# Kernel optimization log

Hardware: AMD Instinct MI355X
Metric: run time of the kernel (lower is better)

The kernel has to match this reference:

```python
import jax, jax.numpy as jnp
import numpy as np

B, S, D, HE, HD = 64, 256, 512, 512, 1024  # batch, seq_len, input_dim, hidden_enc, hidden_dec (=2*HE)


def _gru_cell(h, x, Wih, Whh, bih, bhh):
    # single PyTorch-convention GRU step; gate order [r, z, n]
    H = h.shape[-1]
    gi = x @ Wih.T + bih  # [B, 3H]
    gh = h @ Whh.T + bhh
    r = jax.nn.sigmoid(gi[:, :H] + gh[:, :H])
    z = jax.nn.sigmoid(gi[:, H:2 * H] + gh[:, H:2 * H])
    n = jnp.tanh(gi[:, 2 * H:] + r * gh[:, 2 * H:])
    return (1.0 - z) * n + z * h


def _gru_seq(x, Wih, Whh, bih, bhh):
    # x: [B, S, D] -> outputs [B, S, H], zero initial hidden (torch default)
    h0 = jnp.zeros((x.shape[0], Whh.shape[1]), x.dtype)
    def step(h, xt):
        hn = _gru_cell(h, xt, Wih, Whh, bih, bhh)
        return hn, hn
    _, ys = jax.lax.scan(step, h0, jnp.swapaxes(x, 0, 1))
    return jnp.swapaxes(ys, 0, 1)


def _bigru(x, pf, pb):
    fwd = _gru_seq(x, *pf)
    bwd = _gru_seq(x[:, ::-1], *pb)[:, ::-1]
    return jnp.concatenate([fwd, bwd], axis=-1)  # [B, S, 2H]


def setup_inputs() -> dict:
    key = jax.random.key(0)
    ks = iter(jax.random.split(key, 40))
    f = lambda *shape: (jax.random.normal(next(ks), shape, dtype=jnp.float32) * 0.05)
    inp = {
        'input': f(B, 1, S, D),
        'eps': f(B, S, 2 * HE),
    }
    # encoder mu / sigma bidirectional GRUs (forward + backward directions)
    for name in ['mu_f', 'mu_b', 'sg_f', 'sg_b']:
        inp[name + '_Wih'] = f(3 * HE, D)
        inp[name + '_Whh'] = f(3 * HE, HE)
        inp[name + '_bih'] = f(3 * HE)
        inp[name + '_bhh'] = f(3 * HE)
    # decoder GRU (input_dim -> hidden_dec)
    inp['dec_Wih'] = f(3 * HD, D)
    inp['dec_Whh'] = f(3 * HD, HD)
    inp['dec_bih'] = f(3 * HD)
    inp['dec_bhh'] = f(3 * HD)
    # attention Linear(D+HD, 1) and output Linear(HD, D)
    inp['attn_W'] = f(1, D + HD)
    inp['attn_b'] = f(1)
    inp['lin_W'] = f(D, HD)
    inp['lin_b'] = f(D)
    return inp


def reference(input, eps,
              mu_f_Wih, mu_f_Whh, mu_f_bih, mu_f_bhh,
              mu_b_Wih, mu_b_Whh, mu_b_bih, mu_b_bhh,
              sg_f_Wih, sg_f_Whh, sg_f_bih, sg_f_bhh,
              sg_b_Wih, sg_b_Whh, sg_b_bih, sg_b_bhh,
              dec_Wih, dec_Whh, dec_bih, dec_bhh,
              attn_W, attn_b, lin_W, lin_b):
    x = input[:, 0]  # squeeze -> [B, S, D]
    # encoder (dropout is identity at eval)
    mu = _bigru(x, (mu_f_Wih, mu_f_Whh, mu_f_bih, mu_f_bhh),
                   (mu_b_Wih, mu_b_Whh, mu_b_bih, mu_b_bhh))
    logvar = _bigru(x, (sg_f_Wih, sg_f_Whh, sg_f_bih, sg_f_bhh),
                       (sg_b_Wih, sg_b_Whh, sg_b_bih, sg_b_bhh))
    z = mu + eps * jnp.exp(0.5 * logvar)  # [B, S, HD]

    # attention score = Linear([x_t, hidden]); split into precomputed x-part + per-step hidden part
    sx = x @ attn_W[0, :D] + attn_b[0]  # [B, S]
    wah = attn_W[0, D:]                  # [HD]
    pos = jnp.arange(S)

    def step(carry, i):
        hidden, out = carry  # [B, HD], [B, D]
        scores = sx + (hidden @ wah)[:, None]          # [B, S]
        scores = jnp.where(pos[None, :] == i, -jnp.inf, scores)  # leave-one-out
        w = jax.nn.softmax(scores, axis=1)
        ctx = jnp.einsum('bs,bsh->bh', w, z)           # context = decoder init hidden
        h_new = _gru_cell(ctx, out, dec_Wih, dec_Whh, dec_bih, dec_bhh)
        o_new = h_new @ lin_W.T + lin_b
        return (h_new, o_new), o_new

    h0 = jnp.zeros((B, HD), x.dtype)
    o0 = jnp.zeros((B, D), x.dtype)
    _, rec = jax.lax.scan(step, (h0, o0), pos)
    reconstructed = jnp.swapaxes(rec, 0, 1)  # [B, S, D]
    return reconstructed, mu, logvar
```

## Files before the change

kernel.cpp:

```cpp
#include <hip/hip_runtime.h>
#include <hip/hip_bf16.h>

typedef __hip_bfloat16 bf16;
typedef __attribute__((ext_vector_type(8))) short s8v;
typedef __attribute__((ext_vector_type(4))) float f32x4;
typedef __attribute__((ext_vector_type(4))) int int4v;

#define NB 64
#define NS 256
#define ND 512
#define NHE 512
#define NHD 1024
#define NGE 1536
#define NGD 3072

static __device__ __forceinline__ float sigmf(float x){ return 1.0f/(1.0f+__expf(-x)); }
static __device__ __forceinline__ float b2f(unsigned short u){ return __uint_as_float(((unsigned int)u) << 16); }
static __device__ __forceinline__ unsigned short f2bu(float f){
    bf16 v = __float2bfloat16(f);
    return *reinterpret_cast<unsigned short*>(&v);
}
static __device__ __forceinline__ s8v cast8(int4v v){
    union { int4v i; s8v s; } u; u.i = v; return u.s;
}
static __device__ __forceinline__ void st2_llc(const void* p, unsigned int v){
    asm volatile("global_store_short %0, %1, off sc0 sc1"
                 :: "v"((unsigned long long)(uintptr_t)p), "v"(v) : "memory");
}

#define LOADX8(BASEP, A0,A1,A2,A3,A4,A5,A6,A7)                                   \
    asm volatile(                                                                \
        "global_load_dwordx4 %0, %8, off sc0 sc1\n\t"                            \
        "global_load_dwordx4 %1, %8, off offset:64 sc0 sc1\n\t"                  \
        "global_load_dwordx4 %2, %8, off offset:128 sc0 sc1\n\t"                 \
        "global_load_dwordx4 %3, %8, off offset:192 sc0 sc1\n\t"                 \
        "global_load_dwordx4 %4, %8, off offset:256 sc0 sc1\n\t"                 \
        "global_load_dwordx4 %5, %8, off offset:320 sc0 sc1\n\t"                 \
        "global_load_dwordx4 %6, %8, off offset:384 sc0 sc1\n\t"                 \
        "global_load_dwordx4 %7, %8, off offset:448 sc0 sc1\n\t"                 \
        "s_waitcnt vmcnt(0)"                                                     \
        : "=&v"(A0),"=&v"(A1),"=&v"(A2),"=&v"(A3),                               \
          "=&v"(A4),"=&v"(A5),"=&v"(A6),"=&v"(A7)                                \
        : "v"((unsigned long long)(uintptr_t)(BASEP)) : "memory");               \
    __builtin_amdgcn_sched_barrier(0);

static __device__ __forceinline__ void groupbar_flat(unsigned int* base, int step, int nwg){
    __syncthreads();
    if (threadIdx.x == 0){
        unsigned int old = __hip_atomic_fetch_add(base, 1u, __ATOMIC_RELAXED, __HIP_MEMORY_SCOPE_AGENT);
        if ((int)old == step*nwg - 1)
            __hip_atomic_store(base + 32, (unsigned int)step, __ATOMIC_RELAXED, __HIP_MEMORY_SCOPE_AGENT);
        while ((int)__hip_atomic_load(base + 32, __ATOMIC_RELAXED, __HIP_MEMORY_SCOPE_AGENT) < step)
            __builtin_amdgcn_s_sleep(1);
    }
    __syncthreads();
}
static __device__ __forceinline__ void groupbar_tree(unsigned int* base, int step, int leaf){
    __syncthreads();
    if (threadIdx.x == 0){
        unsigned int lo = __hip_atomic_fetch_add(base + leaf*32, 1u, __ATOMIC_RELAXED, __HIP_MEMORY_SCOPE_AGENT);
        if ((int)lo == step*8 - 1){
            unsigned int ro = __hip_atomic_fetch_add(base + 256, 1u, __ATOMIC_RELAXED, __HIP_MEMORY_SCOPE_AGENT);
            if ((int)ro == step*8 - 1)
                __hip_atomic_store(base + 288, (unsigned int)step, __ATOMIC_RELAXED, __HIP_MEMORY_SCOPE_AGENT);
        }
        while ((int)__hip_atomic_load(base + 288, __ATOMIC_RELAXED, __HIP_MEMORY_SCOPE_AGENT) < step)
            __builtin_amdgcn_s_sleep(1);
    }
    __syncthreads();
}

__global__ __launch_bounds__(256) void k_sx(const float* __restrict__ x,
                                            const float* __restrict__ attnW,
                                            const float* __restrict__ attnb,
                                            float* __restrict__ sx){
    int row = blockIdx.x*4 + (threadIdx.x>>6);
    int lane = threadIdx.x & 63;
    float s = 0.f;
    for (int d = lane; d < ND; d += 64) s += x[(size_t)row*ND + d]*attnW[d];
    #pragma unroll
    for (int off = 32; off; off >>= 1) s += __shfl_down(s, off, 64);
    if (lane == 0) sx[row] = s + attnb[0];
}

__global__ __launch_bounds__(256) void k_cvec(const float* __restrict__ dWih,
                                              const float* __restrict__ linb,
                                              const float* __restrict__ dbih,
                                              float* __restrict__ cvec){
    int row = blockIdx.x*4 + (threadIdx.x>>6);
    int lane = threadIdx.x & 63;
    float s = 0.f;
    for (int d = lane; d < ND; d += 64) s += dWih[(size_t)row*ND + d]*linb[d];
    #pragma unroll
    for (int off = 32; off; off >>= 1) s += __shfl_down(s, off, 64);
    if (lane == 0) cvec[row] = s + dbih[row];
}

__global__ __launch_bounds__(256) void k_softprep2(const float* __restrict__ sx,
                                                   float* __restrict__ esb,
                                                   float* __restrict__ Se){
    int b = blockIdx.x, s = threadIdx.x;
    __shared__ float red[256];
    float v = sx[b*NS + s];
    red[s] = v; __syncthreads();
    for (int off = 128; off; off >>= 1){ if (s < off) red[s] = fmaxf(red[s], red[s+off]); __syncthreads(); }
    float mx = red[0]; __syncthreads();
    float ev = __expf(v - mx);
    esb[s*NB + b] = ev;
    red[s] = ev; __syncthreads();
    for (int off = 128; off; off >>= 1){ if (s < off) red[s] += red[s+off]; __syncthreads(); }
    if (s == 0) Se[b] = red[0];
}

__global__ __launch_bounds__(256) void k_cvtW(const float* __restrict__ W, bf16* __restrict__ o){
    size_t i = ((size_t)blockIdx.x*256 + threadIdx.x)*4;
    float4 v = *(const float4*)(W + i);
    o[i+0] = __float2bfloat16(v.x);
    o[i+1] = __float2bfloat16(v.y);
    o[i+2] = __float2bfloat16(v.z);
    o[i+3] = __float2bfloat16(v.w);
}

__global__ __launch_bounds__(256) void k_zexp3(const bf16* __restrict__ hxh,
                                               const float* __restrict__ eps,
                                               bf16* __restrict__ z){
    int t  = blockIdx.x >> 4;
    int hb = blockIdx.x & 15;
    int dmu = hb >> 3;
    int jm0 = (hb & 7)*64;
    const unsigned short* hu = (const unsigned short*)hxh;
    __shared__ unsigned short zt[64][66];
    int tid = threadIdx.x;
    #pragma unroll
    for (int q = 0; q < 16; ++q){
        int bb = q*4 + (tid>>6);
        int hc = tid & 63;
        float mu = b2f(hu[(((size_t)(dmu*NS) + t)*64 + bb)*512 + jm0 + hc]);
        float lv = b2f(hu[(((size_t)((2+dmu)*NS) + t)*64 + bb)*512 + jm0 + hc]);
        float ep = eps[((size_t)bb*NS + t)*NHD + hb*64 + hc];
        zt[bb][hc] = f2bu(mu + ep*__expf(0.5f*lv));
    }
    __syncthreads();
    unsigned short* zu = (unsigned short*)z;
    int b = tid & 63;
    #pragma unroll
    for (int q = 0; q < 16; ++q){
        int hl = q*4 + (tid>>6);
        zu[((size_t)t*NHD + hb*64 + hl)*NB + b] = zt[b][hl];
    }
}

__global__ __launch_bounds__(256) void k_outT2(const bf16* __restrict__ hxh,
                                               float* __restrict__ outMu,
                                               float* __restrict__ outLv){
    int t  = blockIdx.x;
    int b0 = blockIdx.y*8;
    const unsigned short* hu = (const unsigned short*)hxh;
    int tid = threadIdx.x;
    #pragma unroll
    for (int q = 0; q < 16; ++q){
        int idx = q*256 + tid;
        int sel = idx >> 11;
        int rem = idx & 2047;
        int bb  = b0 + (rem >> 8);
        int h   = (rem & 255)*4;
        int dirn = (h >> 9) + sel*2;
        int j   = h & 511;
        ushort4 v = *(const ushort4*)(hu + (((size_t)(dirn*NS) + t)*64 + bb)*512 + j);
        float4 o;
        o.x = b2f(v.x); o.y = b2f(v.y); o.z = b2f(v.z); o.w = b2f(v.w);
        float* outp = sel ? outLv : outMu;
        *(float4*)(outp + ((size_t)bb*NS + t)*NHD + h) = o;
    }
}

__global__ __launch_bounds__(256) void k_T2(const bf16* __restrict__ z,
                                            const float* __restrict__ esb,
                                            float* __restrict__ T){
    int h = blockIdx.x;
    int b = threadIdx.x & 63;
    int sq = threadIdx.x >> 6;
    __shared__ float red[4][64];
    float acc = 0.f;
    #pragma unroll 8
    for (int s = sq*64; s < sq*64 + 64; ++s)
        acc += esb[s*NB + b]*__bfloat162float(z[((size_t)s*NHD + h)*NB + b]);
    red[sq][b] = acc; __syncthreads();
    if (sq == 0) T[h*NB + b] = red[0][b] + red[1][b] + red[2][b] + red[3][b];
}

__global__ __launch_bounds__(256) void k_ctx3(const bf16* __restrict__ z,
                                              const float* __restrict__ esb,
                                              const float* __restrict__ Se,
                                              const float* __restrict__ T,
                                              bf16* __restrict__ ctxT,
                                              bf16* __restrict__ ctxB){
    int i  = blockIdx.x >> 4;
    int hb = blockIdx.x & 15;
    int tid = threadIdx.x;
    int b  = tid & 63;
    __shared__ unsigned short tt[64][66];
    float ei  = esb[i*NB + b];
    float inv = 1.0f/(Se[b] - ei);
    #pragma unroll
    for (int q = 0; q < 16; ++q){
        int hl = q*4 + (tid>>6);
        int h = hb*64 + hl;
        float zv = __bfloat162float(z[((size_t)i*NHD + h)*NB + b]);
        float cv = (T[h*NB + b] - ei*zv)*inv;
        unsigned short u = f2bu(cv);
        ctxT[((size_t)i*NHD + h)*NB + b] = *reinterpret_cast<bf16*>(&u);
        tt[hl][b] = u;
    }
    __syncthreads();
    unsigned short* cb = (unsigned short*)ctxB;
    #pragma unroll
    for (int q = 0; q < 16; ++q){
        int bn = q*4 + (tid>>6);
        int hl = tid & 63;
        cb[((size_t)i*NB + bn)*NHD + hb*64 + hl] = tt[hl][bn];
    }
}

__global__ __launch_bounds__(256) void k_gemm_M(
    const float* __restrict__ dWih,
    const float* __restrict__ linW,
    bf16* __restrict__ M){
    int g0 = blockIdx.x*64;
    int h0 = blockIdx.y*64;
    __shared__ float As[64][36];
    __shared__ float Bs[32][68];
    int tid = threadIdx.x, tx = tid & 15, ty = tid >> 4;
    float acc[4][4] = {};
    for (int k0 = 0; k0 < ND; k0 += 32){
        #pragma unroll
        for (int m = 0; m < 8; ++m){
            int idx = m*256 + tid;
            int row = idx >> 5, kk = idx & 31;
            As[row][kk] = dWih[(size_t)(g0+row)*ND + k0 + kk];
            int k2 = idx >> 6, hh2 = idx & 63;
            Bs[k2][hh2] = linW[(size_t)(k0+k2)*NHD + h0 + hh2];
        }
        __syncthreads();
        for (int k = 0; k < 32; ++k){
            float a[4];
            #pragma unroll
            for (int i = 0; i < 4; ++i) a[i] = As[ty*4+i][k];
            float4 b4 = *(const float4*)&Bs[k][tx*4];
            #pragma unroll
            for (int i = 0; i < 4; ++i){
                acc[i][0] += a[i]*b4.x; acc[i][1] += a[i]*b4.y;
                acc[i][2] += a[i]*b4.z; acc[i][3] += a[i]*b4.w;
            }
        }
        __syncthreads();
    }
    #pragma unroll
    for (int i = 0; i < 4; ++i)
        #pragma unroll
        for (int j = 0; j < 4; ++j)
            M[(size_t)(g0+ty*4+i)*NHD + h0 + tx*4 + j] = __float2bfloat16(acc[i][j]);
}

__global__ __launch_bounds__(256, 2) void k_xg_mfma(
    const bf16* __restrict__ xb,
    const bf16* __restrict__ WihB,
    const float* __restrict__ b0, const float* __restrict__ b1,
    const float* __restrict__ b2, const float* __restrict__ b3,
    bf16* __restrict__ Xg){
    int t = blockIdx.x, gblk = blockIdx.y, dir = blockIdx.z;
    const float* bih = dir==0?b0:dir==1?b1:dir==2?b2:b3;
    int tid = threadIdx.x;
    int lane = tid & 63;
    int w = __builtin_amdgcn_readfirstlane(tid >> 6);
    int ln = lane & 15, lk = lane >> 4;
    int g = gblk*64 + w*16 + ln;
    const unsigned short* Bp = (const unsigned short*)WihB + ((size_t)(dir*NGE + g))*512 + lk*8;
    s8v Bf[16];
    #pragma unroll
    for (int q = 0; q < 16; ++q) Bf[q] = *(const s8v*)(Bp + q*32);
    f32x4 C[4] = {};
    const unsigned short* xu = (const unsigned short*)xb;
    #pragma unroll
    for (int m = 0; m < 4; ++m){
        const unsigned short* Ap = xu + ((size_t)(m*16+ln)*NS + t)*ND + lk*8;
        #pragma unroll
        for (int q = 0; q < 16; ++q){
            s8v Af = *(const s8v*)(Ap + q*32);
            C[m] = __builtin_amdgcn_mfma_f32_16x16x32_bf16(Af, Bf[q], C[m], 0, 0, 0);
        }
    }
    float bi = bih[g];
    unsigned short* Op = (unsigned short*)Xg + ((size_t)(dir*NS + t)*NGE + g)*NB;
    #pragma unroll
    for (int m = 0; m < 4; ++m){
        ushort4 o;
        o.x = f2bu(C[m][0] + bi); o.y = f2bu(C[m][1] + bi);
        o.z = f2bu(C[m][2] + bi); o.w = f2bu(C[m][3] + bi);
        *(ushort4*)(Op + m*16 + lk*4) = o;
    }
}

__global__ __launch_bounds__(256, 2) void k_gctx_mfma(
    const bf16* __restrict__ ctxB,
    const bf16* __restrict__ dWhhB,
    const float* __restrict__ bhh,
    bf16* __restrict__ Gctx){
    int i = blockIdx.x, gblk = blockIdx.y;
    int tid = threadIdx.x;
    int lane = tid & 63;
    int w = __builtin_amdgcn_readfirstlane(tid >> 6);
    int ln = lane & 15, lk = lane >> 4;
    int g = gblk*64 + w*16 + ln;
    f32x4 C[4] = {};
    const unsigned short* cu = (const unsigned short*)ctxB;
    const unsigned short* wu = (const unsigned short*)dWhhB;
    #pragma unroll
    for (int kc = 0; kc < 2; ++kc){
        const unsigned short* Bp = wu + (size_t)g*NHD + kc*512 + lk*8;
        s8v Bf[16];
        #pragma unroll
        for (int q = 0; q < 16; ++q) Bf[q] = *(const s8v*)(Bp + q*32);
        #pragma unroll
        for (int m = 0; m < 4; ++m){
            const unsigned short* Ap = cu + ((size_t)i*NB + m*16+ln)*NHD + kc*512 + lk*8;
            #pragma unroll
            for (int q = 0; q < 16; ++q){
                s8v Af = *(const s8v*)(Ap + q*32);
                C[m] = __builtin_amdgcn_mfma_f32_16x16x32_bf16(Af, Bf[q], C[m], 0, 0, 0);
            }
        }
    }
    float bi = bhh[g];
    unsigned short* Op = (unsigned short*)Gctx + ((size_t)i*NGD + g)*NB;
    #pragma unroll
    for (int m = 0; m < 4; ++m){
        ushort4 o;
        o.x = f2bu(C[m][0] + bi); o.y = f2bu(C[m][1] + bi);
        o.z = f2bu(C[m][2] + bi); o.w = f2bu(C[m][3] + bi);
        *(ushort4*)(Op + m*16 + lk*4) = o;
    }
}

__global__ __launch_bounds__(256, 2) void k_rec_mfma(
    const bf16* __restrict__ Ht,
    const bf16* __restrict__ linWB,
    const float* __restrict__ linb,
    float* __restrict__ outRec){
    int i = blockIdx.x, dblk = blockIdx.y;
    int tid = threadIdx.x;
    int lane = tid & 63;
    int w = __builtin_amdgcn_readfirstlane(tid >> 6);
    int ln = lane & 15, lk = lane >> 4;
    int d = dblk*64 + w*16 + ln;
    f32x4 C[4] = {};
    const unsigned short* hu = (const unsigned short*)Ht;
    const unsigned short* wu = (const unsigned short*)linWB;
    #pragma unroll
    for (int kc = 0; kc < 2; ++kc){
        const unsigned short* Bp = wu + (size_t)d*NHD + kc*512 + lk*8;
        s8v Bf[16];
        #pragma unroll
        for (int q = 0; q < 16; ++q) Bf[q] = *(const s8v*)(Bp + q*32);
        #pragma unroll
        for (int m = 0; m < 4; ++m){
            const unsigned short* Ap = hu + ((size_t)i*NB + m*16+ln)*NHD + kc*512 + lk*8;
            #pragma unroll
            for (int q = 0; q < 16; ++q){
                s8v Af = *(const s8v*)(Ap + q*32);
                C[m] = __builtin_amdgcn_mfma_f32_16x16x32_bf16(Af, Bf[q], C[m], 0, 0, 0);
            }
        }
    }
    float lb = linb[d];
    #pragma unroll
    for (int m = 0; m < 4; ++m)
        #pragma unroll
        for (int r = 0; r < 4; ++r){
            int b = m*16 + lk*4 + r;
            outRec[((size_t)b*NS + i)*ND + d] = C[m][r] + lb;
        }
}

__global__ __launch_bounds__(256, 1) void k_enc13(
    const bf16* __restrict__ Xg,
    const bf16* __restrict__ WB,
    const float* __restrict__ b0, const float* __restrict__ b1,
    const float* __restrict__ b2, const float* __restrict__ b3,
    bf16* __restrict__ hxh,
    unsigned int* __restrict__ bar){
    int wg  = blockIdx.x;
    int grp = wg & 15;
    int wl  = wg >> 4;
    int dir = grp >> 2;
    int bq  = grp & 3;
    int tid = threadIdx.x;
    int lane = tid & 63;
    int wid = __builtin_amdgcn_readfirstlane(tid >> 6);
    int jl = wid & 1, kh = wid >> 1;
    int jt = wl*2 + jl;
    int ln = lane & 15, lk = lane >> 4;
    int j  = jt*16 + ln;
    int b0v = bq*16 + lk*4;
    const float* bhh = dir==0?b0:dir==1?b1:dir==2?b2:b3;
    const unsigned short* WBu = (const unsigned short*)WB;
    s8v Bf[3][8];
    #pragma unroll
    for (int g = 0; g < 3; ++g)
        #pragma unroll
        for (int q = 0; q < 8; ++q)
            Bf[g][q] = *(const s8v*)(WBu + ((size_t)(dir*NGE + g*512 + j))*512 + (kh*8+q)*32 + lk*8);
    float br=0.f, bz=0.f, bn=0.f;
    if (kh == 0){ br = bhh[j]; bz = bhh[j+512]; bn = bhh[j+1024]; }
    float hp0=0.f, hp1=0.f, hp2=0.f, hp3=0.f;
    __shared__ float red[2][3][64][4];
    unsigned int* gb = bar + grp*64;
    const unsigned short* Xgu = (const unsigned short*)Xg;
    const unsigned short* hu = (const unsigned short*)hxh;
    ushort4 xr, xz, xn;
    if (kh == 0){
        int t0 = (dir & 1) ? 255 : 0;
        size_t xb_ = (size_t)(dir*NS + t0)*NGE;
        xr = *(const ushort4*)(Xgu + (xb_ + j)*NB + b0v);
        xz = *(const ushort4*)(Xgu + (xb_ + j + 512)*NB + b0v);
        xn = *(const ushort4*)(Xgu + (xb_ + j + 1024)*NB + b0v);
    }
    for (int t = 0; t < NS; ++t){
        int tcur = (dir & 1) ? (255 - t) : t;
        f32x4 C0 = {0.f,0.f,0.f,0.f}, C1 = {0.f,0.f,0.f,0.f}, C2 = {0.f,0.f,0.f,0.f};
        if (t > 0){
            int tprev = (dir & 1) ? (256 - t) : (t - 1);
            const unsigned short* hxr = hu
                + (((size_t)(dir*NS + tprev))*64 + bq*16 + ln)*512 + kh*256 + lk*8;
            int4v a0,a1,a2,a3,a4,a5,a6,a7;
            LOADX8(hxr, a0,a1,a2,a3,a4,a5,a6,a7)
            s8v Af;
            #define MF3(AV) Af = cast8(AV); \
                C0 = __builtin_amdgcn_mfma_f32_16x16x32_bf16(Af, Bf[0][__q], C0, 0, 0, 0); \
                C1 = __builtin_amdgcn_mfma_f32_16x16x32_bf16(Af, Bf[1][__q], C1, 0, 0, 0); \
                C2 = __builtin_amdgcn_mfma_f32_16x16x32_bf16(Af, Bf[2][__q], C2, 0, 0, 0);
            { enum {__q=0}; MF3(a0) } { enum {__q=1}; MF3(a1) }
            { enum {__q=2}; MF3(a2) } { enum {__q=3}; MF3(a3) }
            { enum {__q=4}; MF3(a4) } { enum {__q=5}; MF3(a5) }
            { enum {__q=6}; MF3(a6) } { enum {__q=7}; MF3(a7) }
            #undef MF3
        }
        if (kh == 1){
            *(f32x4*)&red[jl][0][lane][0] = C0;
            *(f32x4*)&red[jl][1][lane][0] = C1;
            *(f32x4*)&red[jl][2][lane][0] = C2;
        }
        __syncthreads();
        if (kh == 0){
            C0 += *(const f32x4*)&red[jl][0][lane][0];
            C1 += *(const f32x4*)&red[jl][1][lane][0];
            C2 += *(const f32x4*)&red[jl][2][lane][0];
            {
                float r_ = sigmf(b2f(xr.x) + C0[0] + br);
                float z_ = sigmf(b2f(xz.x) + C1[0] + bz);
                float n_ = tanhf(b2f(xn.x) + r_*(C2[0] + bn));
                hp0 = (1.f - z_)*n_ + z_*hp0;
            }
            {
                float r_ = sigmf(b2f(xr.y) + C0[1] + br);
                float z_ = sigmf(b2f(xz.y) + C1[1] + bz);
                float n_ = tanhf(b2f(xn.y) + r_*(C2[1] + bn));
                hp1 = (1.f - z_)*n_ + z_*hp1;
            }
            {
                float r_ = sigmf(b2f(xr.z) + C0[2] + br);
                float z_ = sigmf(b2f(xz.z) + C1[2] + bz);
                float n_ = tanhf(b2f(xn.z) + r_*(C2[2] + bn));
                hp2 = (1.f - z_)*n_ + z_*hp2;
            }
            {
                float r_ = sigmf(b2f(xr.w) + C0[3] + br);
                float z_ = sigmf(b2f(xz.w) + C1[3] + bz);
                float n_ = tanhf(b2f(xn.w) + r_*(C2[3] + bn));
                hp3 = (1.f - z_)*n_ + z_*hp3;
            }
            const unsigned short* hw = hu + ((size_t)(dir*NS + tcur))*64*512;
            st2_llc(hw + (size_t)(b0v+0)*512 + j, (unsigned int)f2bu(hp0));
            st2_llc(hw + (size_t)(b0v+1)*512 + j, (unsigned int)f2bu(hp1));
            st2_llc(hw + (size_t)(b0v+2)*512 + j, (unsigned int)f2bu(hp2));
            st2_llc(hw + (size_t)(b0v+3)*512 + j, (unsigned int)f2bu(hp3));
            if (t < NS-1){
                int tn = (dir & 1) ? (254 - t) : (t + 1);
                size_t xb_ = (size_t)(dir*NS + tn)*NGE;
                xr = *(const ushort4*)(Xgu + (xb_ + j)*NB + b0v);
                xz = *(const ushort4*)(Xgu + (xb_ + j + 512)*NB + b0v);
                xn = *(const ushort4*)(Xgu + (xb_ + j + 1024)*NB + b0v);
            }
        }
        if (t < NS-1) groupbar_flat(gb, t+1, 16);
    }
}

__global__ __launch_bounds__(256, 1) void k_dec13(
    const bf16* __restrict__ MB,
    const float* __restrict__ cvec,
    const float* __restrict__ dbih,
    const bf16* __restrict__ Gctx,
    const bf16* __restrict__ ctxT,
    bf16* __restrict__ Ht,
    unsigned int* __restrict__ bar){
    int wg  = blockIdx.x;
    int grp = wg & 3;
    int jt  = wg >> 2;
    int tid = threadIdx.x;
    int lane = tid & 63;
    int wid = __builtin_amdgcn_readfirstlane(tid >> 6);
    int ln = lane & 15, lk = lane >> 4;
    int j  = jt*16 + ln;
    int b0v = grp*16 + lk*4;
    const unsigned short* MBu = (const unsigned short*)MB;
    s8v Bf[3][8];
    #pragma unroll
    for (int g = 0; g < 3; ++g)
        #pragma unroll
        for (int q = 0; q < 8; ++q)
            Bf[g][q] = *(const s8v*)(MBu + ((size_t)(g*NHD + j))*NHD + wid*256 + q*32 + lk*8);
    float c0=0.f,c1=0.f,c2=0.f,d0v=0.f,d1v=0.f,d2v=0.f;
    if (wid == 0){
        c0 = cvec[j]; c1 = cvec[j+NHD]; c2 = cvec[j+2*NHD];
        d0v = dbih[j]; d1v = dbih[j+NHD]; d2v = dbih[j+2*NHD];
    }
    __shared__ float red[3][3][64][4];
    unsigned int* gb = bar + grp*512;
    int leaf = jt & 7;
    const unsigned short* Gu = (const unsigned short*)Gctx;
    const unsigned short* Cu = (const unsigned short*)ctxT;
    const unsigned short* hu = (const unsigned short*)Ht;
    ushort4 gr, gz, gn, cx;
    if (wid == 0){
        gr = *(const ushort4*)(Gu + (size_t)j*NB + b0v);
        gz = *(const ushort4*)(Gu + (size_t)(j+NHD)*NB + b0v);
        gn = *(const ushort4*)(Gu + (size_t)(j+2*NHD)*NB + b0v);
        cx = *(const ushort4*)(Cu + (size_t)j*NB + b0v);
    }
    for (int i = 0; i < NS; ++i){
        f32x4 C0 = {0.f,0.f,0.f,0.f}, C1 = {0.f,0.f,0.f,0.f}, C2 = {0.f,0.f,0.f,0.f};
        if (i > 0){
            const unsigned short* hxr = hu
                + ((size_t)(i-1)*NB + grp*16 + ln)*NHD + wid*256 + lk*8;
            int4v a0,a1,a2,a3,a4,a5,a6,a7;
            LOADX8(hxr, a0,a1,a2,a3,a4,a5,a6,a7)
            s8v Af;
            #define MF3(AV) Af = cast8(AV); \
                C0 = __builtin_amdgcn_mfma_f32_16x16x32_bf16(Af, Bf[0][__q], C0, 0, 0, 0); \
                C1 = __builtin_amdgcn_mfma_f32_16x16x32_bf16(Af, Bf[1][__q], C1, 0, 0, 0); \
                C2 = __builtin_amdgcn_mfma_f32_16x16x32_bf16(Af, Bf[2][__q], C2, 0, 0, 0);
            { enum {__q=0}; MF3(a0) } { enum {__q=1}; MF3(a1) }
            { enum {__q=2}; MF3(a2) } { enum {__q=3}; MF3(a3) }
            { enum {__q=4}; MF3(a4) } { enum {__q=5}; MF3(a5) }
            { enum {__q=6}; MF3(a6) } { enum {__q=7}; MF3(a7) }
            #undef MF3
        }
        if (wid != 0){
            *(f32x4*)&red[wid-1][0][lane][0] = C0;
            *(f32x4*)&red[wid-1][1][lane][0] = C1;
            *(f32x4*)&red[wid-1][2][lane][0] = C2;
        }
        __syncthreads();
        if (wid == 0){
            #pragma unroll
            for (int w = 0; w < 3; ++w){
                C0 += *(const f32x4*)&red[w][0][lane][0];
                C1 += *(const f32x4*)&red[w][1][lane][0];
                C2 += *(const f32x4*)&red[w][2][lane][0];
            }
            f32x4 ho;
            {
                float g0v = (i==0) ? d0v : C0[0] + c0;
                float g1v = (i==0) ? d1v : C1[0] + c1;
                float g2v = (i==0) ? d2v : C2[0] + c2;
                float r_ = sigmf(g0v + b2f(gr.x));
                float z_ = sigmf(g1v + b2f(gz.x));
                float n_ = tanhf(g2v + r_*b2f(gn.x));
                ho[0] = (1.f - z_)*n_ + z_*b2f(cx.x);
            }
            {
                float g0v = (i==0) ? d0v : C0[1] + c0;
                float g1v = (i==0) ? d1v : C1[1] + c1;
                float g2v = (i==0) ? d2v : C2[1] + c2;
                float r_ = sigmf(g0v + b2f(gr.y));
                float z_ = sigmf(g1v + b2f(gz.y));
                float n_ = tanhf(g2v + r_*b2f(gn.y));
                ho[1] = (1.f - z_)*n_ + z_*b2f(cx.y);
            }
            {
                float g0v = (i==0) ? d0v : C0[2] + c0;
                float g1v = (i==0) ? d1v : C1[2] + c1;
                float g2v = (i==0) ? d2v : C2[2] + c2;
                float r_ = sigmf(g0v + b2f(gr.z));
                float z_ = sigmf(g1v + b2f(gz.z));
                float n_ = tanhf(g2v + r_*b2f(gn.z));
                ho[2] = (1.f - z_)*n_ + z_*b2f(cx.z);
            }
            {
                float g0v = (i==0) ? d0v : C0[3] + c0;
                float g1v = (i==0) ? d1v : C1[3] + c1;
                float g2v = (i==0) ? d2v : C2[3] + c2;
                float r_ = sigmf(g0v + b2f(gr.w));
                float z_ = sigmf(g1v + b2f(gz.w));
                float n_ = tanhf(g2v + r_*b2f(gn.w));
                ho[3] = (1.f - z_)*n_ + z_*b2f(cx.w);
            }
            const unsigned short* hw = hu + (size_t)i*NB*NHD;
            st2_llc(hw + (size_t)(b0v+0)*NHD + j, (unsigned int)f2bu(ho[0]));
            st2_llc(hw + (size_t)(b0v+1)*NHD + j, (unsigned int)f2bu(ho[1]));
            st2_llc(hw + (size_t)(b0v+2)*NHD + j, (unsigned int)f2bu(ho[2]));
            st2_llc(hw + (size_t)(b0v+3)*NHD + j, (unsigned int)f2bu(ho[3]));
            if (i < NS-1){
                size_t gbx = (size_t)(i+1)*NGD*NB;
                gr = *(const ushort4*)(Gu + gbx + (size_t)j*NB + b0v);
                gz = *(const ushort4*)(Gu + gbx + (size_t)(j+NHD)*NB + b0v);
                gn = *(const ushort4*)(Gu + gbx + (size_t)(j+2*NHD)*NB + b0v);
                cx = *(const ushort4*)(Cu + ((size_t)(i+1)*NHD + j)*NB + b0v);
            }
        }
        if (i < NS-1) groupbar_tree(gb, i+1, leaf);
    }
}

extern "C" void kernel_launch(void* const* d_in, const int* in_sizes, int n_in,
                              void* d_out, int out_size, void* d_ws, size_t ws_size,
                              hipStream_t stream){
    const float* x   = (const float*)d_in[0];
    const float* eps = (const float*)d_in[1];
    const float* Wih[4]; const float* Whh[4]; const float* bih[4]; const float* bhh[4];
    for (int d = 0; d < 4; ++d){
        Wih[d] = (const float*)d_in[2 + 4*d];
        Whh[d] = (const float*)d_in[3 + 4*d];
        bih[d] = (const float*)d_in[4 + 4*d];
        bhh[d] = (const float*)d_in[5 + 4*d];
    }
    const float* dWih  = (const float*)d_in[18];
    const float* dWhh  = (const float*)d_in[19];
    const float* dbih  = (const float*)d_in[20];
    const float* dbhh  = (const float*)d_in[21];
    const float* attnW = (const float*)d_in[22];
    const float* attnb = (const float*)d_in[23];
    const float* linW  = (const float*)d_in[24];
    const float* linb  = (const float*)d_in[25];

    float* out    = (float*)d_out;
    float* outRec = out;
    float* outMu  = out + 8388608;
    float* outLv  = out + 25165824;

    char* ws = (char*)d_ws;
    bf16*  Xg    = (bf16*)(ws + 0);
    bf16*  Gctx  = (bf16*)(ws + 0);
    bf16*  ctxB  = (bf16*)(ws + 100663296);
    bf16*  hxh   = (bf16*)(ws + 201326592);
    bf16*  zbuf  = (bf16*)(ws + 268435456);
    bf16*  ctxT  = (bf16*)(ws + 301989888);
    bf16*  Ht    = (bf16*)(ws + 335544320);
    bf16*  xb    = (bf16*)(ws + 369098752);
    bf16*  WihB  = (bf16*)(ws + 385875968);
    bf16*  WhhB  = (bf16*)(ws + 392167424);
    bf16*  MbufB = (bf16*)(ws + 398458880);
    bf16*  dWhhB = (bf16*)(ws + 404750336);
    bf16*  linWB = (bf16*)(ws + 411041792);
    float* sx    = (float*)(ws + 412090368);
    float* esb   = (float*)(ws + 412155904);
    float* Se    = (float*)(ws + 412221440);
    float* Tbuf  = (float*)(ws + 412225536);
    float* cvec  = (float*)(ws + 412487680);
    unsigned int* barE = (unsigned int*)(ws + 412499968);
    unsigned int* barD = (unsigned int*)(ws + 412516352);

    hipMemsetAsync(ws + 412499968, 0, 32768, stream);

    hipLaunchKernelGGL(k_cvtW, dim3(8192), dim3(256), 0, stream, x, xb);
    for (int d = 0; d < 4; ++d)
        hipLaunchKernelGGL(k_cvtW, dim3(768), dim3(256), 0, stream, Wih[d], WihB + (size_t)d*NGE*NHE);
    for (int d = 0; d < 4; ++d)
        hipLaunchKernelGGL(k_cvtW, dim3(768), dim3(256), 0, stream, Whh[d], WhhB + (size_t)d*NGE*NHE);
    hipLaunchKernelGGL(k_gemm_M, dim3(48,16), dim3(256), 0, stream, dWih, linW, MbufB);
    hipLaunchKernelGGL(k_cvec, dim3(768), dim3(256), 0, stream, dWih, linb, dbih, cvec);
    hipLaunchKernelGGL(k_sx, dim3(4096), dim3(256), 0, stream, x, attnW, attnb, sx);
    hipLaunchKernelGGL(k_softprep2, dim3(64), dim3(256), 0, stream, sx, esb, Se);
    hipLaunchKernelGGL(k_xg_mfma, dim3(256,24,4), dim3(256), 0, stream,
                       xb, WihB, bih[0], bih[1], bih[2], bih[3], Xg);

    {
        void* a[] = { (void*)&Xg, (void*)&WhhB,
                      (void*)&bhh[0], (void*)&bhh[1], (void*)&bhh[2], (void*)&bhh[3],
                      (void*)&hxh, (void*)&barE };
        hipLaunchCooperativeKernel((void*)k_enc13, dim3(256), dim3(256), a, 0, stream);
    }

    hipLaunchKernelGGL(k_zexp3, dim3(4096), dim3(256), 0, stream, hxh, eps, zbuf);
    hipLaunchKernelGGL(k_outT2, dim3(256,8), dim3(256), 0, stream, hxh, outMu, outLv);
    hipLaunchKernelGGL(k_cvtW, dim3(3072), dim3(256), 0, stream, dWhh, dWhhB);
    hipLaunchKernelGGL(k_cvtW, dim3(512), dim3(256), 0, stream, linW, linWB);
    hipLaunchKernelGGL(k_T2, dim3(1024), dim3(256), 0, stream, zbuf, esb, Tbuf);
    hipLaunchKernelGGL(k_ctx3, dim3(4096), dim3(256), 0, stream, zbuf, esb, Se, Tbuf, ctxT, ctxB);
    hipLaunchKernelGGL(k_gctx_mfma, dim3(256,48), dim3(256), 0, stream, ctxB, dWhhB, dbhh, Gctx);

    {
        void* a[] = { (void*)&MbufB, (void*)&cvec, (void*)&dbih, (void*)&Gctx, (void*)&ctxT,
                      (void*)&Ht, (void*)&barD };
        hipLaunchCooperativeKernel((void*)k_dec13, dim3(256), dim3(256), a, 0, stream);
    }

    hipLaunchKernelGGL(k_rec_mfma, dim3(256,8), dim3(256), 0, stream, Ht, linWB, linb, outRec);
}
```

Measured before the change: 3.906 ms.

## Simplify grid barriers, batch weight conversions, and double per-block timesteps in GEMMs

The grid barriers now spin directly on the arrival counter, where before a separate release flag was written by the last arriver. This removes one dependent atomic round-trip per step in the serial encoder and decoder loops. The eight weight-conversion launches are merged into two 2D-grid launches. The input-gate and context-gate MFMA kernels now process two timesteps per block, so weight fragments loaded into registers are reused across both. That halves the grid size, which may lower occupancy or raise register pressure.

```diff
diff --git a/kernel.cpp b/kernel.cpp
--- a/kernel.cpp
+++ b/kernel.cpp
@@ -47,10 +47,8 @@
 static __device__ __forceinline__ void groupbar_flat(unsigned int* base, int step, int nwg){
     __syncthreads();
     if (threadIdx.x == 0){
-        unsigned int old = __hip_atomic_fetch_add(base, 1u, __ATOMIC_RELAXED, __HIP_MEMORY_SCOPE_AGENT);
-        if ((int)old == step*nwg - 1)
-            __hip_atomic_store(base + 32, (unsigned int)step, __ATOMIC_RELAXED, __HIP_MEMORY_SCOPE_AGENT);
-        while ((int)__hip_atomic_load(base + 32, __ATOMIC_RELAXED, __HIP_MEMORY_SCOPE_AGENT) < step)
+        __hip_atomic_fetch_add(base, 1u, __ATOMIC_RELAXED, __HIP_MEMORY_SCOPE_AGENT);
+        while ((int)__hip_atomic_load(base, __ATOMIC_RELAXED, __HIP_MEMORY_SCOPE_AGENT) < step*nwg)
             __builtin_amdgcn_s_sleep(1);
     }
     __syncthreads();
@@ -59,12 +57,9 @@
     __syncthreads();
     if (threadIdx.x == 0){
         unsigned int lo = __hip_atomic_fetch_add(base + leaf*32, 1u, __ATOMIC_RELAXED, __HIP_MEMORY_SCOPE_AGENT);
-        if ((int)lo == step*8 - 1){
-            unsigned int ro = __hip_atomic_fetch_add(base + 256, 1u, __ATOMIC_RELAXED, __HIP_MEMORY_SCOPE_AGENT);
-            if ((int)ro == step*8 - 1)
-                __hip_atomic_store(base + 288, (unsigned int)step, __ATOMIC_RELAXED, __HIP_MEMORY_SCOPE_AGENT);
-        }
-        while ((int)__hip_atomic_load(base + 288, __ATOMIC_RELAXED, __HIP_MEMORY_SCOPE_AGENT) < step)
+        if ((int)lo == step*8 - 1)
+            __hip_atomic_fetch_add(base + 256, 1u, __ATOMIC_RELAXED, __HIP_MEMORY_SCOPE_AGENT);
+        while ((int)__hip_atomic_load(base + 256, __ATOMIC_RELAXED, __HIP_MEMORY_SCOPE_AGENT) < step*8)
             __builtin_amdgcn_s_sleep(1);
     }
     __syncthreads();
@@ -121,6 +116,21 @@
     o[i+3] = __float2bfloat16(v.w);
 }
 
+__global__ __launch_bounds__(256) void k_cvtW4(
+    const float* __restrict__ p0, const float* __restrict__ p1,
+    const float* __restrict__ p2, const float* __restrict__ p3,
+    bf16* __restrict__ o){
+    int y = blockIdx.y;
+    const float* W = (y==0)?p0:(y==1)?p1:(y==2)?p2:p3;
+    size_t i = ((size_t)blockIdx.x*256 + threadIdx.x)*4;
+    float4 v = *(const float4*)(W + i);
+    bf16* d = o + (size_t)y*NGE*NHE;
+    d[i+0] = __float2bfloat16(v.x);
+    d[i+1] = __float2bfloat16(v.y);
+    d[i+2] = __float2bfloat16(v.z);
+    d[i+3] = __float2bfloat16(v.w);
+}
+
 __global__ __launch_bounds__(256) void k_zexp3(const bf16* __restrict__ hxh,
                                                const float* __restrict__ eps,
                                                bf16* __restrict__ z){
@@ -262,13 +272,13 @@
             M[(size_t)(g0+ty*4+i)*NHD + h0 + tx*4 + j] = __float2bfloat16(acc[i][j]);
 }
 
-__global__ __launch_bounds__(256, 2) void k_xg_mfma(
+__global__ __launch_bounds__(256, 2) void k_xg_mfma2(
     const bf16* __restrict__ xb,
     const bf16* __restrict__ WihB,
     const float* __restrict__ b0, const float* __restrict__ b1,
     const float* __restrict__ b2, const float* __restrict__ b3,
     bf16* __restrict__ Xg){
-    int t = blockIdx.x, gblk = blockIdx.y, dir = blockIdx.z;
+    int t0 = blockIdx.x*2, gblk = blockIdx.y, dir = blockIdx.z;
     const float* bih = dir==0?b0:dir==1?b1:dir==2?b2:b3;
     int tid = threadIdx.x;
     int lane = tid & 63;
@@ -279,40 +289,43 @@
     s8v Bf[16];
     #pragma unroll
     for (int q = 0; q < 16; ++q) Bf[q] = *(const s8v*)(Bp + q*32);
-    f32x4 C[4] = {};
+    float bi = bih[g];
     const unsigned short* xu = (const unsigned short*)xb;
-    #pragma unroll
-    for (int m = 0; m < 4; ++m){
-        const unsigned short* Ap = xu + ((size_t)(m*16+ln)*NS + t)*ND + lk*8;
-        #pragma unroll
-        for (int q = 0; q < 16; ++q){
-            s8v Af = *(const s8v*)(Ap + q*32);
-            C[m] = __builtin_amdgcn_mfma_f32_16x16x32_bf16(Af, Bf[q], C[m], 0, 0, 0);
-        }
-    }
-    float bi = bih[g];
-    unsigned short* Op = (unsigned short*)Xg + ((size_t)(dir*NS + t)*NGE + g)*NB;
-    #pragma unroll
-    for (int m = 0; m < 4; ++m){
-        ushort4 o;
-        o.x = f2bu(C[m][0] + bi); o.y = f2bu(C[m][1] + bi);
-        o.z = f2bu(C[m][2] + bi); o.w = f2bu(C[m][3] + bi);
-        *(ushort4*)(Op + m*16 + lk*4) = o;
-    }
-}
-
-__global__ __launch_bounds__(256, 2) void k_gctx_mfma(
+    for (int tt = 0; tt < 2; ++tt){
+        int t = t0 + tt;
+        f32x4 C[4] = {};
+        #pragma unroll
+        for (int m = 0; m < 4; ++m){
+            const unsigned short* Ap = xu + ((size_t)(m*16+ln)*NS + t)*ND + lk*8;
+            #pragma unroll
+            for (int q = 0; q < 16; ++q){
+                s8v Af = *(const s8v*)(Ap + q*32);
+                C[m] = __builtin_amdgcn_mfma_f32_16x16x32_bf16(Af, Bf[q], C[m], 0, 0, 0);
+            }
+        }
+        unsigned short* Op = (unsigned short*)Xg + ((size_t)(dir*NS + t)*NGE + g)*NB;
+        #pragma unroll
+        for (int m = 0; m < 4; ++m){
+            ushort4 o;
+            o.x = f2bu(C[m][0] + bi); o.y = f2bu(C[m][1] + bi);
+            o.z = f2bu(C[m][2] + bi); o.w = f2bu(C[m][3] + bi);
+            *(ushort4*)(Op + m*16 + lk*4) = o;
+        }
+    }
+}
+
+__global__ __launch_bounds__(256, 2) void k_gctx_mfma2(
     const bf16* __restrict__ ctxB,
     const bf16* __restrict__ dWhhB,
     const float* __restrict__ bhh,
     bf16* __restrict__ Gctx){
-    int i = blockIdx.x, gblk = blockIdx.y;
+    int i0 = blockIdx.x*2, gblk = blockIdx.y;
     int tid = threadIdx.x;
     int lane = tid & 63;
     int w = __builtin_amdgcn_readfirstlane(tid >> 6);
     int ln = lane & 15, lk = lane >> 4;
     int g = gblk*64 + w*16 + ln;
-    f32x4 C[4] = {};
+    f32x4 C[2][4] = {};
     const unsigned short* cu = (const unsigned short*)ctxB;
     const unsigned short* wu = (const unsigned short*)dWhhB;
     #pragma unroll
@@ -322,23 +335,29 @@
         #pragma unroll
         for (int q = 0; q < 16; ++q) Bf[q] = *(const s8v*)(Bp + q*32);
         #pragma unroll
+        for (int ii = 0; ii < 2; ++ii){
+            #pragma unroll
+            for (int m = 0; m < 4; ++m){
+                const unsigned short* Ap = cu + ((size_t)(i0+ii)*NB + m*16+ln)*NHD + kc*512 + lk*8;
+                #pragma unroll
+                for (int q = 0; q < 16; ++q){
+                    s8v Af = *(const s8v*)(Ap + q*32);
+                    C[ii][m] = __builtin_amdgcn_mfma_f32_16x16x32_bf16(Af, Bf[q], C[ii][m], 0, 0, 0);
+                }
+            }
+        }
+    }
+    float bi = bhh[g];
+    #pragma unroll
+    for (int ii = 0; ii < 2; ++ii){
+        unsigned short* Op = (unsigned short*)Gctx + ((size_t)(i0+ii)*NGD + g)*NB;
+        #pragma unroll
         for (int m = 0; m < 4; ++m){
-            const unsigned short* Ap = cu + ((size_t)i*NB + m*16+ln)*NHD + kc*512 + lk*8;
-            #pragma unroll
-            for (int q = 0; q < 16; ++q){
-                s8v Af = *(const s8v*)(Ap + q*32);
-                C[m] = __builtin_amdgcn_mfma_f32_16x16x32_bf16(Af, Bf[q], C[m], 0, 0, 0);
-            }
-        }
-    }
-    float bi = bhh[g];
-    unsigned short* Op = (unsigned short*)Gctx + ((size_t)i*NGD + g)*NB;
-    #pragma unroll
-    for (int m = 0; m < 4; ++m){
-        ushort4 o;
-        o.x = f2bu(C[m][0] + bi); o.y = f2bu(C[m][1] + bi);
-        o.z = f2bu(C[m][2] + bi); o.w = f2bu(C[m][3] + bi);
-        *(ushort4*)(Op + m*16 + lk*4) = o;
+            ushort4 o;
+            o.x = f2bu(C[ii][m][0] + bi); o.y = f2bu(C[ii][m][1] + bi);
+            o.z = f2bu(C[ii][m][2] + bi); o.w = f2bu(C[ii][m][3] + bi);
+            *(ushort4*)(Op + m*16 + lk*4) = o;
+        }
     }
 }
 
@@ -382,7 +401,7 @@
         }
 }
 
-__global__ __launch_bounds__(256, 1) void k_enc13(
+__global__ __launch_bounds__(256, 1) void k_enc14(
     const bf16* __restrict__ Xg,
     const bf16* __restrict__ WB,
     const float* __restrict__ b0, const float* __restrict__ b1,
@@ -496,7 +515,7 @@
     }
 }
 
-__global__ __launch_bounds__(256, 1) void k_dec13(
+__global__ __launch_bounds__(256, 1) void k_dec14(
     const bf16* __restrict__ MB,
     const float* __restrict__ cvec,
     const float* __restrict__ dbih,
@@ -674,22 +693,22 @@
     hipMemsetAsync(ws + 412499968, 0, 32768, stream);
 
     hipLaunchKernelGGL(k_cvtW, dim3(8192), dim3(256), 0, stream, x, xb);
-    for (int d = 0; d < 4; ++d)
-        hipLaunchKernelGGL(k_cvtW, dim3(768), dim3(256), 0, stream, Wih[d], WihB + (size_t)d*NGE*NHE);
-    for (int d = 0; d < 4; ++d)
-        hipLaunchKernelGGL(k_cvtW, dim3(768), dim3(256), 0, stream, Whh[d], WhhB + (size_t)d*NGE*NHE);
+    hipLaunchKernelGGL(k_cvtW4, dim3(768,4), dim3(256), 0, stream,
+                       Wih[0], Wih[1], Wih[2], Wih[3], WihB);
+    hipLaunchKernelGGL(k_cvtW4, dim3(768,4), dim3(256), 0, stream,
+                       Whh[0], Whh[1], Whh[2], Whh[3], WhhB);
     hipLaunchKernelGGL(k_gemm_M, dim3(48,16), dim3(256), 0, stream, dWih, linW, MbufB);
     hipLaunchKernelGGL(k_cvec, dim3(768), dim3(256), 0, stream, dWih, linb, dbih, cvec);
     hipLaunchKernelGGL(k_sx, dim3(4096), dim3(256), 0, stream, x, attnW, attnb, sx);
     hipLaunchKernelGGL(k_softprep2, dim3(64), dim3(256), 0, stream, sx, esb, Se);
-    hipLaunchKernelGGL(k_xg_mfma, dim3(256,24,4), dim3(256), 0, stream,
+    hipLaunchKernelGGL(k_xg_mfma2, dim3(128,24,4), dim3(256), 0, stream,
                        xb, WihB, bih[0], bih[1], bih[2], bih[3], Xg);
 
     {
         void* a[] = { (void*)&Xg, (void*)&WhhB,
                       (void*)&bhh[0], (void*)&bhh[1], (void*)&bhh[2], (void*)&bhh[3],
                       (void*)&hxh, (void*)&barE };
-        hipLaunchCooperativeKernel((void*)k_enc13, dim3(256), dim3(256), a, 0, stream);
+        hipLaunchCooperativeKernel((void*)k_enc14, dim3(256), dim3(256), a, 0, stream);
     }
 
     hipLaunchKernelGGL(k_zexp3, dim3(4096), dim3(256), 0, stream, hxh, eps, zbuf);
@@ -698,12 +717,12 @@
     hipLaunchKernelGGL(k_cvtW, dim3(512), dim3(256), 0, stream, linW, linWB);
     hipLaunchKernelGGL(k_T2, dim3(1024), dim3(256), 0, stream, zbuf, esb, Tbuf);
     hipLaunchKernelGGL(k_ctx3, dim3(4096), dim3(256), 0, stream, zbuf, esb, Se, Tbuf, ctxT, ctxB);
-    hipLaunchKernelGGL(k_gctx_mfma, dim3(256,48), dim3(256), 0, stream, ctxB, dWhhB, dbhh, Gctx);
+    hipLaunchKernelGGL(k_gctx_mfma2, dim3(128,48), dim3(256), 0, stream, ctxB, dWhhB, dbhh, Gctx);
 
     {
         void* a[] = { (void*)&MbufB, (void*)&cvec, (void*)&dbih, (void*)&Gctx, (void*)&ctxT,
                       (void*)&Ht, (void*)&barD };
-        hipLaunchCooperativeKernel((void*)k_dec13, dim3(256), dim3(256), a, 0, stream);
+        hipLaunchCooperativeKernel((void*)k_dec14, dim3(256), dim3(256), a, 0, stream);
     }
 
     hipLaunchKernelGGL(k_rec_mfma, dim3(256,8), dim3(256), 0, stream, Ht, linWB, linb, outRec);
```

Result: faster. 3.658 ms (-6.3%).
